# Performance work log

Measured on AMD Instinct MI355X. Metric: run time of the kernel, lower is better.

## Reference

```python
import jax, jax.numpy as jnp
import numpy as np


def _euclidean_cdist(x, q):
    # torch.cdist with p=2: pairwise L2 distances, shape [B, Q]
    x2 = jnp.sum(x * x, axis=-1, keepdims=True)          # [B, 1]
    q2 = jnp.sum(q * q, axis=-1)[None, :]                # [1, Q]
    d2 = x2 + q2 - 2.0 * (x @ q.T)                        # [B, Q]
    return jnp.sqrt(jnp.maximum(d2, 0.0))


def setup_inputs() -> dict:
    key = jax.random.key(0)
    k1, k2 = jax.random.split(key)
    x = jax.random.normal(k1, (1024, 256), dtype=jnp.float32)
    queue = jax.random.normal(k2, (32768, 256), dtype=jnp.float32)
    return {"x": x, "queue": queue}


def reference(x, queue):
    # Queue update: concat then keep the newest max_size rows (queue assumed full)
    max_size = queue.shape[0]
    q = jnp.concatenate([queue, x], axis=0)[-max_size:]   # [Q, F]
    # Distance matrix + top-2 nearest (topk of negated distances)
    d = _euclidean_cdist(x, q)                            # [B, Q]
    _, idx = jax.lax.top_k(-d, 2)                         # [B, 2]
    # Second-nearest neighbor (first is the point itself, dist 0)
    return q[idx[:, 1]]                                   # [B, F]
```

## Files before the change

kernel.cpp:

```cpp
#include <hip/hip_runtime.h>
#include <stdint.h>

#define B_ROWS 1024
#define FEAT   256
#define QSZ    32768
#define SHIFT  1024
#define QX     (QSZ - B_ROWS)
#define NQB    256
#define NXB    8
#define MARGIN 8.0f

typedef float  v4f __attribute__((ext_vector_type(4)));
typedef short  v8s __attribute__((ext_vector_type(8)));

__device__ __forceinline__ uint32_t key_flip(uint32_t u) {
    return u ^ ((uint32_t)((int32_t)u >> 31) | 0x80000000u);
}
__device__ __forceinline__ float key_m(uint32_t k) {
    uint32_t u = k & 0xFFFF8000u;
    u = (u & 0x80000000u) ? (u ^ 0x80000000u) : ~u;
    return __uint_as_float(u);
}
__device__ __forceinline__ void k2_insert(uint32_t& k1, uint32_t& k2, uint32_t key) {
    uint32_t hi = max(k1, key); k1 = min(k1, key); k2 = min(k2, hi);
}
__device__ __forceinline__ uint2 k2_merge(uint2 a, uint2 b) {
    uint32_t hi = max(a.x, b.x);
    uint2 r; r.x = min(a.x, b.x); r.y = min(min(a.y, b.y), hi);
    return r;
}

struct Top2 { float m1; int j1; float m2; int j2; };
__device__ __forceinline__ bool better(float ma, int ja, float mb, int jb) {
    return (ma < mb) || (ma == mb && ja < jb);
}
__device__ __forceinline__ void t2_insert(Top2& t, float m, int j) {
    if (better(m, j, t.m1, t.j1)) { t.m2 = t.m1; t.j2 = t.j1; t.m1 = m; t.j1 = j; }
    else if (better(m, j, t.m2, t.j2)) { t.m2 = m; t.j2 = j; }
}

__device__ __forceinline__ const float* q_row_ptr(int j, const float* x, const float* queue) {
    return (j < QX) ? (queue + (size_t)(j + SHIFT) * FEAT) : (x + (size_t)(j - QX) * FEAT);
}

__device__ __forceinline__ unsigned short f2bf(float f) {
    uint32_t u = __float_as_uint(f);
    uint32_t r = u + 0x7FFFu + ((u >> 16) & 1u);
    return (unsigned short)(r >> 16);
}

__device__ __forceinline__ void lds_load16(const void* g, void* l) {
    __builtin_amdgcn_global_load_lds(
        (const __attribute__((address_space(1))) uint32_t*)g,
        (__attribute__((address_space(3))) uint32_t*)l, 16, 0, 0);
}

__global__ __launch_bounds__(256) void convert_kernel(const float* __restrict__ x,
                                                      const float* __restrict__ queue,
                                                      unsigned short* __restrict__ q_bf,
                                                      float* __restrict__ q2) {
    int wave = threadIdx.x >> 6, lane = threadIdx.x & 63;
    int j = blockIdx.x * 4 + wave;
    const float4* row = (const float4*)q_row_ptr(j, x, queue);
    float4 v = row[lane];
    float s = v.x * v.x + v.y * v.y + v.z * v.z + v.w * v.w;
#pragma unroll
    for (int off = 32; off; off >>= 1) s += __shfl_xor(s, off, 64);
    if (lane == 0) q2[j] = s;
    ushort4 h;
    h.x = f2bf(v.x); h.y = f2bf(v.y); h.z = f2bf(v.z); h.w = f2bf(v.w);
    ((ushort4*)q_bf)[(size_t)j * 64 + lane] = h;
}

__global__ __launch_bounds__(256, 3) void nn_mfma(const unsigned short* __restrict__ q_bf,
                                                  const float* __restrict__ q2,
                                                  uint2* __restrict__ partials) {
    __shared__ unsigned short As[128 * 64];
    __shared__ unsigned short Bs[128 * 64];
    __shared__ float sq2[128];
    __shared__ uint2 scr[128][2];

    const int t    = threadIdx.x;
    const int w    = t >> 6, lane = t & 63;
    const int wm   = w >> 1, wn = w & 1;
    const int quad = lane >> 4, l16 = lane & 15;
    const int gy   = blockIdx.x;
    const int gx   = blockIdx.y;

    const unsigned short* x_bf = q_bf + (size_t)QX * FEAT;

    if (t < 128) sq2[t] = q2[gy * 128 + t];

    v4f acc[4][4];
#pragma unroll
    for (int a = 0; a < 4; ++a)
#pragma unroll
        for (int b = 0; b < 4; ++b) acc[a][b] = (v4f)0.0f;

    const int srow = lane >> 3;
    const int sg   = (lane & 7) ^ srow;

    for (int c = 0; c < 4; ++c) {
        __syncthreads();
#pragma unroll
        for (int kk = 0; kk < 4; ++kk) {
            int row = w * 32 + kk * 8 + srow;
            const unsigned short* ga = q_bf + (size_t)(gy * 128 + row) * FEAT + c * 64 + sg * 8;
            const unsigned short* gb = x_bf + (size_t)(gx * 128 + row) * FEAT + c * 64 + sg * 8;
            lds_load16(ga, &As[(w * 32 + kk * 8) * 64]);
            lds_load16(gb, &Bs[(w * 32 + kk * 8) * 64]);
        }
        __syncthreads();
#pragma unroll
        for (int ks = 0; ks < 2; ++ks) {
            v8s fa[4], fb[4];
            const int goff  = (((ks * 4 + quad) ^ (l16 & 7)) << 4);
            const int abase = (wm * 64 + l16) * 128 + goff;
            const int bbase = (wn * 64 + l16) * 128 + goff;
#pragma unroll
            for (int tm = 0; tm < 4; ++tm)
                fa[tm] = *(const v8s*)((const char*)As + abase + tm * 2048);
#pragma unroll
            for (int tn = 0; tn < 4; ++tn)
                fb[tn] = *(const v8s*)((const char*)Bs + bbase + tn * 2048);
#pragma unroll
            for (int tm = 0; tm < 4; ++tm)
#pragma unroll
                for (int tn = 0; tn < 4; ++tn)
                    acc[tm][tn] = __builtin_amdgcn_mfma_f32_16x16x32_bf16(fa[tm], fb[tn], acc[tm][tn], 0, 0, 0);
        }
    }

    float q2r[4][4];
#pragma unroll
    for (int tm = 0; tm < 4; ++tm) {
        v4f qq = *(const v4f*)&sq2[wm * 64 + tm * 16 + quad * 4];
#pragma unroll
        for (int r = 0; r < 4; ++r) q2r[tm][r] = qq[r];
    }
    const int jbase = gy * 128 + wm * 64 + quad * 4;

    uint2 best[4];
#pragma unroll
    for (int tn = 0; tn < 4; ++tn) {
        uint32_t k1 = 0xFFFFFFFFu, k2 = 0xFFFFFFFFu;
#pragma unroll
        for (int tm = 0; tm < 4; ++tm)
#pragma unroll
            for (int r = 0; r < 4; ++r) {
                float m = fmaf(-2.0f, acc[tm][tn][r], q2r[tm][r]);
                uint32_t u = key_flip(__float_as_uint(m));
                uint32_t key = (u & 0xFFFF8000u) | (uint32_t)(jbase + tm * 16 + r);
                k2_insert(k1, k2, key);
            }
#pragma unroll
        for (int mask = 16; mask <= 32; mask <<= 1) {
            uint32_t o1 = __shfl_xor(k1, mask, 64);
            uint32_t o2 = __shfl_xor(k2, mask, 64);
            uint32_t hi = max(k1, o1);
            k1 = min(k1, o1);
            k2 = min(min(k2, o2), hi);
        }
        best[tn] = make_uint2(k1, k2);
    }
    if (quad == 0) {
#pragma unroll
        for (int tn = 0; tn < 4; ++tn) scr[wn * 64 + tn * 16 + l16][wm] = best[tn];
    }
    __syncthreads();
    if (t < 128) {
        uint2 r = k2_merge(scr[t][0], scr[t][1]);
        partials[(size_t)(gx * 128 + t) * NQB + gy] = r;
    }
}

__global__ __launch_bounds__(256) void nn_finalize(const float* __restrict__ x,
                                                   const float* __restrict__ queue,
                                                   const float* __restrict__ q2,
                                                   const uint2* __restrict__ partials,
                                                   float* __restrict__ out) {
    __shared__ float    xs[256];
    __shared__ uint2    red[256];
    __shared__ int      list[64];
    __shared__ float    escore[64];
    __shared__ int      s_cnt;
    __shared__ uint32_t s_kcut;
    __shared__ int      s_j2;

    const int t = threadIdx.x, i = blockIdx.x;
    const int w = t >> 6, lane = t & 63;

    xs[t] = x[(size_t)i * FEAT + t];
    uint2 p = partials[(size_t)i * NQB + t];
    red[t] = p;
    if (t == 0) s_cnt = 0;
    __syncthreads();

    if (w == 0) {
        uint2 a = red[lane];
        a = k2_merge(a, red[lane + 64]);
        a = k2_merge(a, red[lane + 128]);
        a = k2_merge(a, red[lane + 192]);
#pragma unroll
        for (int mask = 1; mask <= 32; mask <<= 1) {
            uint2 o;
            o.x = __shfl_xor(a.x, mask, 64);
            o.y = __shfl_xor(a.y, mask, 64);
            a = k2_merge(a, o);
        }
        if (lane == 0) {
            float cutf = key_m(a.y) + MARGIN;
            s_kcut = key_flip(__float_as_uint(cutf)) | 0x7FFFu;
        }
    }
    __syncthreads();
    uint32_t kcut = s_kcut;
    if (p.x <= kcut) { int q_ = atomicAdd(&s_cnt, 1); if (q_ < 64) list[q_] = (int)(p.x & 0x7FFFu); }
    if (p.y <= kcut) { int q_ = atomicAdd(&s_cnt, 1); if (q_ < 64) list[q_] = (int)(p.y & 0x7FFFu); }
    __syncthreads();
    int n = min(s_cnt, 64);

    for (int c = w; c < n; c += 4) {
        int j = list[c];
        const float4* qr = (const float4*)q_row_ptr(j, x, queue);
        float4 qv = qr[lane];
        float4 xv = ((const float4*)xs)[lane];
        float s = qv.x * xv.x + qv.y * xv.y + qv.z * xv.z + qv.w * xv.w;
#pragma unroll
        for (int off = 32; off; off >>= 1) s += __shfl_xor(s, off, 64);
        if (lane == 0) escore[c] = q2[j] - 2.0f * s;
    }
    __syncthreads();
    if (t == 0) {
        Top2 a;
        a.m1 = __builtin_inff(); a.j1 = 0x7FFFFFFF;
        a.m2 = __builtin_inff(); a.j2 = 0x7FFFFFFF;
        for (int c = 0; c < n; ++c) t2_insert(a, escore[c], list[c]);
        s_j2 = a.j2;
    }
    __syncthreads();
    out[(size_t)i * FEAT + t] = q_row_ptr(s_j2, x, queue)[t];
}

extern "C" void kernel_launch(void* const* d_in, const int* in_sizes, int n_in,
                              void* d_out, int out_size, void* d_ws, size_t ws_size,
                              hipStream_t stream) {
    const float* x     = (const float*)d_in[0];
    const float* queue = (const float*)d_in[1];

    unsigned short* q_bf     = (unsigned short*)d_ws;
    float*          q2       = (float*)((char*)d_ws + (16u << 20));
    uint2*          partials = (uint2*)((char*)d_ws + (17u << 20));

    convert_kernel<<<QSZ / 4, 256, 0, stream>>>(x, queue, q_bf, q2);
    nn_mfma<<<dim3(NQB, NXB), 256, 0, stream>>>(q_bf, q2, partials);
    nn_finalize<<<B_ROWS, 256, 0, stream>>>(x, queue, q2, partials, (float*)d_out);
}
```

Measured before the change: 111.9 us.

## Switch candidate GEMM to FP8 scaled MFMA and slim finalize to one wave

The candidate-screening GEMM now converts the queue and x to FP8 instead of BF16 and uses the 16x16x128 scaled f8f6f4 MFMA. This halves staging bytes and the number of K iterations. The rescoring margin grows to absorb the larger FP8 error, so more candidates may be rescored in fp32. The finalize kernel becomes a single-wave block that keeps partials in registers and rescores candidates serially, which drops the block-wide syncs and shared-memory reductions.

```diff
diff --git a/kernel.cpp b/kernel.cpp
--- a/kernel.cpp
+++ b/kernel.cpp
@@ -8,10 +8,11 @@
 #define QX     (QSZ - B_ROWS)
 #define NQB    256
 #define NXB    8
-#define MARGIN 8.0f
-
-typedef float  v4f __attribute__((ext_vector_type(4)));
-typedef short  v8s __attribute__((ext_vector_type(8)));
+#define MARGIN 20.0f
+
+typedef float v4f __attribute__((ext_vector_type(4)));
+typedef int   v4i __attribute__((ext_vector_type(4)));
+typedef int   v8i __attribute__((ext_vector_type(8)));
 
 __device__ __forceinline__ uint32_t key_flip(uint32_t u) {
     return u ^ ((uint32_t)((int32_t)u >> 31) | 0x80000000u);
@@ -43,12 +44,6 @@
     return (j < QX) ? (queue + (size_t)(j + SHIFT) * FEAT) : (x + (size_t)(j - QX) * FEAT);
 }
 
-__device__ __forceinline__ unsigned short f2bf(float f) {
-    uint32_t u = __float_as_uint(f);
-    uint32_t r = u + 0x7FFFu + ((u >> 16) & 1u);
-    return (unsigned short)(r >> 16);
-}
-
 __device__ __forceinline__ void lds_load16(const void* g, void* l) {
     __builtin_amdgcn_global_load_lds(
         (const __attribute__((address_space(1))) uint32_t*)g,
@@ -57,7 +52,7 @@
 
 __global__ __launch_bounds__(256) void convert_kernel(const float* __restrict__ x,
                                                       const float* __restrict__ queue,
-                                                      unsigned short* __restrict__ q_bf,
+                                                      uint32_t* __restrict__ q_f8,
                                                       float* __restrict__ q2) {
     int wave = threadIdx.x >> 6, lane = threadIdx.x & 63;
     int j = blockIdx.x * 4 + wave;
@@ -67,16 +62,16 @@
 #pragma unroll
     for (int off = 32; off; off >>= 1) s += __shfl_xor(s, off, 64);
     if (lane == 0) q2[j] = s;
-    ushort4 h;
-    h.x = f2bf(v.x); h.y = f2bf(v.y); h.z = f2bf(v.z); h.w = f2bf(v.w);
-    ((ushort4*)q_bf)[(size_t)j * 64 + lane] = h;
-}
-
-__global__ __launch_bounds__(256, 3) void nn_mfma(const unsigned short* __restrict__ q_bf,
+    uint32_t u = __builtin_amdgcn_cvt_pk_fp8_f32(v.x, v.y, 0, false);
+    u = __builtin_amdgcn_cvt_pk_fp8_f32(v.z, v.w, u, true);
+    q_f8[(size_t)j * 64 + lane] = u;
+}
+
+__global__ __launch_bounds__(256, 3) void nn_mfma(const uint8_t* __restrict__ q_f8,
                                                   const float* __restrict__ q2,
                                                   uint2* __restrict__ partials) {
-    __shared__ unsigned short As[128 * 64];
-    __shared__ unsigned short Bs[128 * 64];
+    __shared__ uint8_t As[128 * 128];
+    __shared__ uint8_t Bs[128 * 128];
     __shared__ float sq2[128];
     __shared__ uint2 scr[128][2];
 
@@ -87,7 +82,7 @@
     const int gy   = blockIdx.x;
     const int gx   = blockIdx.y;
 
-    const unsigned short* x_bf = q_bf + (size_t)QX * FEAT;
+    const uint8_t* x_f8 = q_f8 + (size_t)QX * FEAT;
 
     if (t < 128) sq2[t] = q2[gy * 128 + t];
 
@@ -99,36 +94,47 @@
 
     const int srow = lane >> 3;
     const int sg   = (lane & 7) ^ srow;
-
-    for (int c = 0; c < 4; ++c) {
+    const int gsw  = l16 & 7;
+    const int g0   = (2 * quad) ^ gsw;
+    const int g1   = (2 * quad + 1) ^ gsw;
+
+    for (int c = 0; c < 2; ++c) {
         __syncthreads();
 #pragma unroll
         for (int kk = 0; kk < 4; ++kk) {
             int row = w * 32 + kk * 8 + srow;
-            const unsigned short* ga = q_bf + (size_t)(gy * 128 + row) * FEAT + c * 64 + sg * 8;
-            const unsigned short* gb = x_bf + (size_t)(gx * 128 + row) * FEAT + c * 64 + sg * 8;
-            lds_load16(ga, &As[(w * 32 + kk * 8) * 64]);
-            lds_load16(gb, &Bs[(w * 32 + kk * 8) * 64]);
+            const uint8_t* ga = q_f8 + (size_t)(gy * 128 + row) * FEAT + c * 128 + sg * 16;
+            const uint8_t* gb = x_f8 + (size_t)(gx * 128 + row) * FEAT + c * 128 + sg * 16;
+            lds_load16(ga, &As[(w * 32 + kk * 8) * 128]);
+            lds_load16(gb, &Bs[(w * 32 + kk * 8) * 128]);
         }
         __syncthreads();
-#pragma unroll
-        for (int ks = 0; ks < 2; ++ks) {
-            v8s fa[4], fb[4];
-            const int goff  = (((ks * 4 + quad) ^ (l16 & 7)) << 4);
-            const int abase = (wm * 64 + l16) * 128 + goff;
-            const int bbase = (wn * 64 + l16) * 128 + goff;
-#pragma unroll
-            for (int tm = 0; tm < 4; ++tm)
-                fa[tm] = *(const v8s*)((const char*)As + abase + tm * 2048);
+        const uint8_t* arow = As + (wm * 64 + l16) * 128;
+        const uint8_t* brow = Bs + (wn * 64 + l16) * 128;
+        v8i fa[4], fb[4];
+#pragma unroll
+        for (int tm = 0; tm < 4; ++tm) {
+            v4i lo = *(const v4i*)(arow + tm * 2048 + g0 * 16);
+            v4i hi = *(const v4i*)(arow + tm * 2048 + g1 * 16);
+            fa[tm][0] = lo[0]; fa[tm][1] = lo[1]; fa[tm][2] = lo[2]; fa[tm][3] = lo[3];
+            fa[tm][4] = hi[0]; fa[tm][5] = hi[1]; fa[tm][6] = hi[2]; fa[tm][7] = hi[3];
+        }
+#pragma unroll
+        for (int tn = 0; tn < 4; ++tn) {
+            v4i lo = *(const v4i*)(brow + tn * 2048 + g0 * 16);
+            v4i hi = *(const v4i*)(brow + tn * 2048 + g1 * 16);
+            fb[tn][0] = lo[0]; fb[tn][1] = lo[1]; fb[tn][2] = lo[2]; fb[tn][3] = lo[3];
+            fb[tn][4] = hi[0]; fb[tn][5] = hi[1]; fb[tn][6] = hi[2]; fb[tn][7] = hi[3];
+        }
+#pragma unroll
+        for (int tm = 0; tm < 4; ++tm)
 #pragma unroll
             for (int tn = 0; tn < 4; ++tn)
-                fb[tn] = *(const v8s*)((const char*)Bs + bbase + tn * 2048);
-#pragma unroll
-            for (int tm = 0; tm < 4; ++tm)
-#pragma unroll
-                for (int tn = 0; tn < 4; ++tn)
-                    acc[tm][tn] = __builtin_amdgcn_mfma_f32_16x16x32_bf16(fa[tm], fb[tn], acc[tm][tn], 0, 0, 0);
-        }
+                acc[tm][tn] = __builtin_amdgcn_mfma_scale_f32_16x16x128_f8f6f4(
+                    fa[tm], fb[tn], acc[tm][tn],
+                    0, 0,
+                    0, 0x7F7F7F7F,
+                    0, 0x7F7F7F7F);
     }
 
     float q2r[4][4];
@@ -174,72 +180,56 @@
     }
 }
 
-__global__ __launch_bounds__(256) void nn_finalize(const float* __restrict__ x,
-                                                   const float* __restrict__ queue,
-                                                   const float* __restrict__ q2,
-                                                   const uint2* __restrict__ partials,
-                                                   float* __restrict__ out) {
-    __shared__ float    xs[256];
-    __shared__ uint2    red[256];
-    __shared__ int      list[64];
-    __shared__ float    escore[64];
-    __shared__ int      s_cnt;
-    __shared__ uint32_t s_kcut;
-    __shared__ int      s_j2;
-
-    const int t = threadIdx.x, i = blockIdx.x;
-    const int w = t >> 6, lane = t & 63;
-
-    xs[t] = x[(size_t)i * FEAT + t];
-    uint2 p = partials[(size_t)i * NQB + t];
-    red[t] = p;
-    if (t == 0) s_cnt = 0;
-    __syncthreads();
-
-    if (w == 0) {
-        uint2 a = red[lane];
-        a = k2_merge(a, red[lane + 64]);
-        a = k2_merge(a, red[lane + 128]);
-        a = k2_merge(a, red[lane + 192]);
-#pragma unroll
-        for (int mask = 1; mask <= 32; mask <<= 1) {
-            uint2 o;
-            o.x = __shfl_xor(a.x, mask, 64);
-            o.y = __shfl_xor(a.y, mask, 64);
-            a = k2_merge(a, o);
-        }
-        if (lane == 0) {
-            float cutf = key_m(a.y) + MARGIN;
-            s_kcut = key_flip(__float_as_uint(cutf)) | 0x7FFFu;
-        }
-    }
-    __syncthreads();
-    uint32_t kcut = s_kcut;
-    if (p.x <= kcut) { int q_ = atomicAdd(&s_cnt, 1); if (q_ < 64) list[q_] = (int)(p.x & 0x7FFFu); }
-    if (p.y <= kcut) { int q_ = atomicAdd(&s_cnt, 1); if (q_ < 64) list[q_] = (int)(p.y & 0x7FFFu); }
+__global__ __launch_bounds__(64) void nn_finalize(const float* __restrict__ x,
+                                                  const float* __restrict__ queue,
+                                                  const float* __restrict__ q2,
+                                                  const uint2* __restrict__ partials,
+                                                  float* __restrict__ out) {
+    __shared__ int list[64];
+    __shared__ int s_cnt;
+
+    const int i = blockIdx.x, lane = threadIdx.x;
+    if (lane == 0) s_cnt = 0;
+
+    const uint2* p = partials + (size_t)i * NQB;
+    uint2 mine[4];
+#pragma unroll
+    for (int u = 0; u < 4; ++u) mine[u] = p[lane + 64 * u];
+    uint2 a = k2_merge(k2_merge(mine[0], mine[1]), k2_merge(mine[2], mine[3]));
+#pragma unroll
+    for (int mask = 1; mask <= 32; mask <<= 1) {
+        uint2 o;
+        o.x = __shfl_xor(a.x, mask, 64);
+        o.y = __shfl_xor(a.y, mask, 64);
+        a = k2_merge(a, o);
+    }
+    float cutf = key_m(a.y) + MARGIN;
+    uint32_t kcut = key_flip(__float_as_uint(cutf)) | 0x7FFFu;
+
+#pragma unroll
+    for (int u = 0; u < 4; ++u) {
+        if (mine[u].x <= kcut) list[atomicAdd(&s_cnt, 1) & 63] = (int)(mine[u].x & 0x7FFFu);
+        if (mine[u].y <= kcut) list[atomicAdd(&s_cnt, 1) & 63] = (int)(mine[u].y & 0x7FFFu);
+    }
     __syncthreads();
     int n = min(s_cnt, 64);
 
-    for (int c = w; c < n; c += 4) {
+    float4 xv = ((const float4*)(x + (size_t)i * FEAT))[lane];
+    Top2 bst;
+    bst.m1 = __builtin_inff(); bst.j1 = 0x7FFFFFFF;
+    bst.m2 = __builtin_inff(); bst.j2 = 0x7FFFFFFF;
+    for (int c = 0; c < n; ++c) {
         int j = list[c];
-        const float4* qr = (const float4*)q_row_ptr(j, x, queue);
-        float4 qv = qr[lane];
-        float4 xv = ((const float4*)xs)[lane];
+        float4 qv = ((const float4*)q_row_ptr(j, x, queue))[lane];
         float s = qv.x * xv.x + qv.y * xv.y + qv.z * xv.z + qv.w * xv.w;
 #pragma unroll
         for (int off = 32; off; off >>= 1) s += __shfl_xor(s, off, 64);
-        if (lane == 0) escore[c] = q2[j] - 2.0f * s;
-    }
-    __syncthreads();
-    if (t == 0) {
-        Top2 a;
-        a.m1 = __builtin_inff(); a.j1 = 0x7FFFFFFF;
-        a.m2 = __builtin_inff(); a.j2 = 0x7FFFFFFF;
-        for (int c = 0; c < n; ++c) t2_insert(a, escore[c], list[c]);
-        s_j2 = a.j2;
-    }
-    __syncthreads();
-    out[(size_t)i * FEAT + t] = q_row_ptr(s_j2, x, queue)[t];
+        float m = q2[j] - 2.0f * s;
+        t2_insert(bst, m, j);
+    }
+    int j2 = bst.j2;
+    float4 o = ((const float4*)q_row_ptr(j2, x, queue))[lane];
+    ((float4*)(out + (size_t)i * FEAT))[lane] = o;
 }
 
 extern "C" void kernel_launch(void* const* d_in, const int* in_sizes, int n_in,
@@ -248,11 +238,11 @@
     const float* x     = (const float*)d_in[0];
     const float* queue = (const float*)d_in[1];
 
-    unsigned short* q_bf     = (unsigned short*)d_ws;
-    float*          q2       = (float*)((char*)d_ws + (16u << 20));
-    uint2*          partials = (uint2*)((char*)d_ws + (17u << 20));
-
-    convert_kernel<<<QSZ / 4, 256, 0, stream>>>(x, queue, q_bf, q2);
-    nn_mfma<<<dim3(NQB, NXB), 256, 0, stream>>>(q_bf, q2, partials);
-    nn_finalize<<<B_ROWS, 256, 0, stream>>>(x, queue, q2, partials, (float*)d_out);
-}
+    uint32_t* q_f8     = (uint32_t*)d_ws;
+    float*    q2       = (float*)((char*)d_ws + (8u << 20));
+    uint2*    partials = (uint2*)((char*)d_ws + (9u << 20));
+
+    convert_kernel<<<QSZ / 4, 256, 0, stream>>>(x, queue, q_f8, q2);
+    nn_mfma<<<dim3(NQB, NXB), 256, 0, stream>>>((const uint8_t*)q_f8, q2, partials);
+    nn_finalize<<<B_ROWS, 64, 0, stream>>>(x, queue, q2, partials, (float*)d_out);
+}
```

Result: slower. 120.2 us (+7.4%).
